# Kernel optimization log

Hardware: AMD Instinct MI355X
Metric: run time of the kernel (lower is better)

## Reference

```python
import jax, jax.numpy as jnp
import numpy as np

X_MIN, X_MAX = -3.0, 3.0
EPS = 1e-08


def setup_inputs() -> dict:
    key = jax.random.key(0)
    k1, k2, k3 = jax.random.split(key, 3)
    B, D_in, D_out, K = 8192, 512, 128, 16
    x = jax.random.normal(k1, (B, D_in), dtype=jnp.float32)
    # trunc_normal_(std=0.02) approximated by scaled normal
    weights = jax.random.normal(k2, (D_out, D_in, K), dtype=jnp.float32) * 0.02
    # xavier_uniform for skip
    limit = float(np.sqrt(6.0 / (D_in + D_out)))
    skip_w = jax.random.uniform(k3, (D_out, D_in), dtype=jnp.float32,
                                minval=-limit, maxval=limit)
    bias = jnp.zeros((D_out,), dtype=jnp.float32)
    return {"x": x, "weights": weights, "skip_w": skip_w, "bias": bias}


def reference(x, weights, skip_w, bias):
    # x: (B, D_in); weights: (D_out, D_in, K); skip_w: (D_out, D_in); bias: (D_out,)
    K = weights.shape[-1]
    t = jnp.clip((x - X_MIN) / (X_MAX - X_MIN + EPS), 0.0, 1.0)
    pos = t * (K - 1)
    idx0 = jnp.floor(pos).astype(jnp.int32)
    idx1 = jnp.minimum(idx0 + 1, K - 1)
    frac = jnp.clip(pos - idx0.astype(pos.dtype), 0.0, 1.0)
    # Hat-basis coefficients per (b, i): avoids materializing (B, D_out, D_in)
    oh0 = jax.nn.one_hot(idx0, K, dtype=x.dtype)  # (B, D_in, K)
    oh1 = jax.nn.one_hot(idx1, K, dtype=x.dtype)
    c = oh0 * (1.0 - frac)[..., None] + oh1 * frac[..., None]  # (B, D_in, K)
    # y[b,o] = sum_i (1-frac)*w[o,i,idx0] + frac*w[o,i,idx1]
    y = jnp.einsum('bik,oik->bo', c, weights)
    y = y + bias + x @ skip_w.T
    return y
```

## Files before the change

kernel.cpp:

```cpp
#include <hip/hip_runtime.h>

typedef __attribute__((ext_vector_type(8))) short short8;
typedef __attribute__((ext_vector_type(4))) float f32x4;

#define DIN 512
#define DOUT 128
#define KK 16
#define BTOT 8192
#define KAUG (DIN * KK + DIN)
#define BK 64
#define NCHUNK_TOT (KAUG / BK)
#define NSPL 8
#define CPB (NCHUNK_TOT / NSPL)
#define BM 128
#define CHUNK_BYTES (DOUT * BK * 2)
#define CBASE 32768
#define LDS_BYTES 65536

__device__ static inline unsigned short f2bf(float x) {
  unsigned u = __builtin_bit_cast(unsigned, x);
  return (unsigned short)((u + 0x7FFFu + ((u >> 16) & 1u)) >> 16);
}

__device__ static inline void llds16(const char* g, char* l) {
  __builtin_amdgcn_global_load_lds(
      (const __attribute__((address_space(1))) unsigned int*)g,
      (__attribute__((address_space(3))) unsigned int*)l, 16, 0, 0);
}

__global__ __launch_bounds__(256) void build_wpp(const float* __restrict__ w,
                                                 const float* __restrict__ sk,
                                                 unsigned short* __restrict__ wpp) {
  const int gi = blockIdx.x * 256 + threadIdx.x;
  const int g = gi >> 10;
  const int rem = gi & 1023;
  const int o = rem >> 3;
  const int kcs = rem & 7;
  const int kc = kcs ^ (o & 7);
  const int kglob = g * 64 + kc * 8;
  const float* src = (kglob < 8192) ? (w + (size_t)o * 8192 + kglob)
                                    : (sk + (size_t)o * 512 + (kglob - 8192));
  const float4 v0 = ((const float4*)src)[0];
  const float4 v1 = ((const float4*)src)[1];
  uint4 pk;
  pk.x = f2bf(v0.x) | ((unsigned)f2bf(v0.y) << 16);
  pk.y = f2bf(v0.z) | ((unsigned)f2bf(v0.w) << 16);
  pk.z = f2bf(v1.x) | ((unsigned)f2bf(v1.y) << 16);
  pk.w = f2bf(v1.z) | ((unsigned)f2bf(v1.w) << 16);
  ((uint4*)wpp)[gi] = pk;
}

__global__ __launch_bounds__(256, 2) void kan_mfma(const float* __restrict__ x,
                                                   const unsigned short* __restrict__ wpp,
                                                   const float* __restrict__ bias,
                                                   float* __restrict__ out) {
  __shared__ __align__(16) char smem[LDS_BYTES];
  const int tid = threadIdx.x;
  const int bt = blockIdx.x >> 3;
  const int sp = blockIdx.x & 7;
  const int b0 = bt * BM;
  const int wid = tid >> 6, lane = tid & 63;
  const int lr = lane & 15, lq = lane >> 4;
  const int wm = wid >> 1, wn = wid & 1;
  const int g0 = sp * CPB;

  f32x4 acc[4][4] = {};

  auto stageW = [&](int g, int buf) {
    const char* gsrc = ((const char*)wpp) + (size_t)g * CHUNK_BYTES + wid * 4096 + lane * 16;
    char* ldst = smem + buf + wid * 4096;
#pragma unroll
    for (int it = 0; it < 4; ++it) llds16(gsrc + it * 1024, ldst + it * 1024);
  };

  auto buildSpline = [&](int cbuf, float xv0, float xv1) {
#pragma unroll
    for (int hh = 0; hh < 2; ++hh) {
      const int bl = (tid >> 2) + hh * 64;
      const int il = tid & 3;
      const float xv = hh ? xv1 : xv0;
      float t = fminf(fmaxf((xv + 3.0f) * (1.0f / 6.0f), 0.0f), 1.0f);
      const float pos = t * 15.0f;
      int i0 = (int)pos;
      i0 = i0 > 14 ? 14 : i0;
      const float f = pos - (float)i0;
      char* row = smem + cbuf + bl * 128;
      const int swz = bl & 7;
      char* gA = row + (((il * 2) ^ swz) << 4);
      char* gB = row + (((il * 2 + 1) ^ swz) << 4);
      *(uint4*)gA = make_uint4(0, 0, 0, 0);
      *(uint4*)gB = make_uint4(0, 0, 0, 0);
      const unsigned short h0 = f2bf(1.0f - f);
      const unsigned short h1 = f2bf(f);
      const int i1 = i0 + 1;
      *(unsigned short*)(((i0 & 8) ? gB : gA) + (i0 & 7) * 2) = h0;
      *(unsigned short*)(((i1 & 8) ? gB : gA) + (i1 & 7) * 2) = h1;
    }
  };

  auto buildSkip = [&](int g, int cbuf) {
    const int ioff = (g - 128) * BK;
    const int bl = tid >> 1, q = tid & 1;
    const float* xr = x + (size_t)(b0 + bl) * DIN + ioff;
    char* row = smem + cbuf + bl * 128;
    const int swz = bl & 7;
#pragma unroll
    for (int gg = 0; gg < 4; ++gg) {
      const int kc = q * 4 + gg;
      const float4 v0 = ((const float4*)(xr + kc * 8))[0];
      const float4 v1 = ((const float4*)(xr + kc * 8))[1];
      uint4 pk;
      pk.x = f2bf(v0.x) | ((unsigned)f2bf(v0.y) << 16);
      pk.y = f2bf(v0.z) | ((unsigned)f2bf(v0.w) << 16);
      pk.z = f2bf(v1.x) | ((unsigned)f2bf(v1.y) << 16);
      pk.w = f2bf(v1.z) | ((unsigned)f2bf(v1.w) << 16);
      *(uint4*)(row + ((kc ^ swz) << 4)) = pk;
    }
  };

  auto loadX = [&](int g, float& a, float& b) {
    const int r0 = tid >> 2, il = tid & 3;
    a = x[(size_t)(b0 + r0) * DIN + g * 4 + il];
    b = x[(size_t)(b0 + 64 + r0) * DIN + g * 4 + il];
  };

  stageW(g0, 0);
  {
    float a, b;
    loadX(g0, a, b);
    buildSpline(CBASE + 0, a, b);
  }
  __syncthreads();

  for (int c = 0; c < CPB; ++c) {
    const int g = g0 + c;
    const int pb = (c & 1) << 14;
    const int nb = pb ^ 16384;
    const bool haveNext = (c + 1 < CPB);
    const int gn = g + 1;

    float xn0 = 0.0f, xn1 = 0.0f;
    if (haveNext && gn < 128) loadX(gn, xn0, xn1);
    if (haveNext) stageW(gn, nb);

    const char* Wb = smem + pb;
    const char* Cb = smem + CBASE + pb;
#pragma unroll
    for (int ks = 0; ks < 2; ++ks) {
      const int gq = ks * 4 + lq;
      short8 af[4], bfr[4];
#pragma unroll
      for (int mt = 0; mt < 4; ++mt) {
        const int m = wm * 64 + mt * 16 + lr;
        af[mt] = *(const short8*)(Cb + m * 128 + ((gq ^ (m & 7)) << 4));
      }
#pragma unroll
      for (int nt = 0; nt < 4; ++nt) {
        const int o = wn * 64 + nt * 16 + lr;
        bfr[nt] = *(const short8*)(Wb + o * 128 + ((gq ^ (o & 7)) << 4));
      }
#pragma unroll
      for (int mt = 0; mt < 4; ++mt)
#pragma unroll
        for (int nt = 0; nt < 4; ++nt)
          acc[mt][nt] = __builtin_amdgcn_mfma_f32_16x16x32_bf16(af[mt], bfr[nt], acc[mt][nt], 0, 0, 0);
    }

    if (haveNext) {
      if (gn < 128) buildSpline(CBASE + nb, xn0, xn1);
      else buildSkip(gn, CBASE + nb);
    }
    __syncthreads();
  }

#pragma unroll
  for (int nt = 0; nt < 4; ++nt) {
    const int col = wn * 64 + nt * 16 + lr;
    const float bv = (sp == 0) ? bias[col] : 0.0f;
#pragma unroll
    for (int mt = 0; mt < 4; ++mt) {
      const int rowb = b0 + wm * 64 + mt * 16 + lq * 4;
#pragma unroll
      for (int r = 0; r < 4; ++r)
        atomicAdd(out + (size_t)(rowb + r) * DOUT + col, acc[mt][nt][r] + bv);
    }
  }
}

__global__ void kan_naive(const float* __restrict__ x, const float* __restrict__ w,
                          const float* __restrict__ skw, const float* __restrict__ bias,
                          float* __restrict__ out) {
  const int b = blockIdx.x;
  const int o = threadIdx.x;
  float acc = bias[o];
  for (int i = 0; i < DIN; ++i) {
    float xv = x[(size_t)b * DIN + i];
    float t = fminf(fmaxf((xv + 3.0f) * (1.0f / 6.0f), 0.0f), 1.0f);
    float p = t * 15.0f;
    float fi = floorf(p);
    int i0 = (int)fi;
    int i1 = (i0 < 15) ? i0 + 1 : 15;
    float f = p - fi;
    const float* wr = &w[((size_t)o * DIN + i) * KK];
    acc += (1.0f - f) * wr[i0] + f * wr[i1] + xv * skw[(size_t)o * DIN + i];
  }
  out[(size_t)b * DOUT + o] = acc;
}

extern "C" void kernel_launch(void* const* d_in, const int* in_sizes, int n_in,
                              void* d_out, int out_size, void* d_ws, size_t ws_size,
                              hipStream_t stream) {
  const float* x    = (const float*)d_in[0];
  const float* w    = (const float*)d_in[1];
  const float* skw  = (const float*)d_in[2];
  const float* bias = (const float*)d_in[3];
  float* out = (float*)d_out;

  const size_t need = (size_t)NCHUNK_TOT * CHUNK_BYTES;
  if (ws_size < need) {
    kan_naive<<<BTOT, DOUT, 0, stream>>>(x, w, skw, bias, out);
    return;
  }

  unsigned short* wpp = (unsigned short*)d_ws;

  hipMemsetAsync(d_out, 0, (size_t)out_size * sizeof(float), stream);
  build_wpp<<<NCHUNK_TOT * 1024 / 256, 256, 0, stream>>>(w, skw, wpp);
  kan_mfma<<<(BTOT / BM) * NSPL, 256, 0, stream>>>(x, wpp, bias, out);
}
```

Before: 120.2 us.

## Load weight fragments directly from global into registers, shrink batch tile

Removes LDS staging of the weight chunk via global_load_lds. Each wave now reads its B fragments straight from a re-laid-out global buffer, with the weight layout changed to kq-major so lanes read contiguous 16-byte pieces. The batch tile is halved to 64 rows with 128-thread blocks, which doubles the block count and halves LDS use. Block order is changed so that splits sharing the same weight chunk run adjacently, and the atomic output columns are rotated per split to reduce contention. In exchange, the weights are fetched from global/L2 more often and global load latency is exposed inside the loop with no prefetch.

```diff
diff --git a/kernel.cpp b/kernel.cpp
--- a/kernel.cpp
+++ b/kernel.cpp
@@ -12,20 +12,14 @@
 #define NCHUNK_TOT (KAUG / BK)
 #define NSPL 8
 #define CPB (NCHUNK_TOT / NSPL)
-#define BM 128
+#define BM 64
 #define CHUNK_BYTES (DOUT * BK * 2)
-#define CBASE 32768
-#define LDS_BYTES 65536
+#define CT_BYTES (BM * BK * 2)
+#define LDS_BYTES (2 * CT_BYTES)
 
 __device__ static inline unsigned short f2bf(float x) {
   unsigned u = __builtin_bit_cast(unsigned, x);
   return (unsigned short)((u + 0x7FFFu + ((u >> 16) & 1u)) >> 16);
-}
-
-__device__ static inline void llds16(const char* g, char* l) {
-  __builtin_amdgcn_global_load_lds(
-      (const __attribute__((address_space(1))) unsigned int*)g,
-      (__attribute__((address_space(3))) unsigned int*)l, 16, 0, 0);
 }
 
 __global__ __launch_bounds__(256) void build_wpp(const float* __restrict__ w,
@@ -34,10 +28,9 @@
   const int gi = blockIdx.x * 256 + threadIdx.x;
   const int g = gi >> 10;
   const int rem = gi & 1023;
-  const int o = rem >> 3;
-  const int kcs = rem & 7;
-  const int kc = kcs ^ (o & 7);
-  const int kglob = g * 64 + kc * 8;
+  const int kq = rem >> 7;
+  const int o = rem & 127;
+  const int kglob = g * 64 + kq * 8;
   const float* src = (kglob < 8192) ? (w + (size_t)o * 8192 + kglob)
                                     : (sk + (size_t)o * 512 + (kglob - 8192));
   const float4 v0 = ((const float4*)src)[0];
@@ -50,33 +43,26 @@
   ((uint4*)wpp)[gi] = pk;
 }
 
-__global__ __launch_bounds__(256, 2) void kan_mfma(const float* __restrict__ x,
+__global__ __launch_bounds__(128, 2) void kan_mfma(const float* __restrict__ x,
                                                    const unsigned short* __restrict__ wpp,
                                                    const float* __restrict__ bias,
                                                    float* __restrict__ out) {
   __shared__ __align__(16) char smem[LDS_BYTES];
   const int tid = threadIdx.x;
-  const int bt = blockIdx.x >> 3;
-  const int sp = blockIdx.x & 7;
+  const int sp = blockIdx.x >> 7;
+  const int bt = blockIdx.x & 127;
   const int b0 = bt * BM;
-  const int wid = tid >> 6, lane = tid & 63;
+  const int wn = tid >> 6;
+  const int lane = tid & 63;
   const int lr = lane & 15, lq = lane >> 4;
-  const int wm = wid >> 1, wn = wid & 1;
   const int g0 = sp * CPB;
 
   f32x4 acc[4][4] = {};
 
-  auto stageW = [&](int g, int buf) {
-    const char* gsrc = ((const char*)wpp) + (size_t)g * CHUNK_BYTES + wid * 4096 + lane * 16;
-    char* ldst = smem + buf + wid * 4096;
-#pragma unroll
-    for (int it = 0; it < 4; ++it) llds16(gsrc + it * 1024, ldst + it * 1024);
-  };
-
   auto buildSpline = [&](int cbuf, float xv0, float xv1) {
 #pragma unroll
     for (int hh = 0; hh < 2; ++hh) {
-      const int bl = (tid >> 2) + hh * 64;
+      const int bl = (tid >> 2) + hh * 32;
       const int il = tid & 3;
       const float xv = hh ? xv1 : xv0;
       float t = fminf(fmaxf((xv + 3.0f) * (1.0f / 6.0f), 0.0f), 1.0f);
@@ -106,80 +92,86 @@
     const int swz = bl & 7;
 #pragma unroll
     for (int gg = 0; gg < 4; ++gg) {
-      const int kc = q * 4 + gg;
-      const float4 v0 = ((const float4*)(xr + kc * 8))[0];
-      const float4 v1 = ((const float4*)(xr + kc * 8))[1];
+      const int kq = q * 4 + gg;
+      const float4 v0 = ((const float4*)(xr + kq * 8))[0];
+      const float4 v1 = ((const float4*)(xr + kq * 8))[1];
       uint4 pk;
       pk.x = f2bf(v0.x) | ((unsigned)f2bf(v0.y) << 16);
       pk.y = f2bf(v0.z) | ((unsigned)f2bf(v0.w) << 16);
       pk.z = f2bf(v1.x) | ((unsigned)f2bf(v1.y) << 16);
       pk.w = f2bf(v1.z) | ((unsigned)f2bf(v1.w) << 16);
-      *(uint4*)(row + ((kc ^ swz) << 4)) = pk;
+      *(uint4*)(row + ((kq ^ swz) << 4)) = pk;
     }
   };
 
   auto loadX = [&](int g, float& a, float& b) {
     const int r0 = tid >> 2, il = tid & 3;
     a = x[(size_t)(b0 + r0) * DIN + g * 4 + il];
-    b = x[(size_t)(b0 + 64 + r0) * DIN + g * 4 + il];
+    b = x[(size_t)(b0 + 32 + r0) * DIN + g * 4 + il];
   };
 
-  stageW(g0, 0);
   {
     float a, b;
     loadX(g0, a, b);
-    buildSpline(CBASE + 0, a, b);
+    buildSpline(0, a, b);
   }
   __syncthreads();
 
   for (int c = 0; c < CPB; ++c) {
     const int g = g0 + c;
-    const int pb = (c & 1) << 14;
-    const int nb = pb ^ 16384;
+    const int pb = (c & 1) << 13;
+    const int nb = pb ^ 8192;
     const bool haveNext = (c + 1 < CPB);
     const int gn = g + 1;
 
+    short8 bfr[4][2];
+    {
+      const char* gb = ((const char*)wpp) + (size_t)g * CHUNK_BYTES;
+#pragma unroll
+      for (int nt = 0; nt < 4; ++nt)
+#pragma unroll
+        for (int ks = 0; ks < 2; ++ks) {
+          const int kq = ks * 4 + lq;
+          const int o = wn * 64 + nt * 16 + lr;
+          bfr[nt][ks] = *(const short8*)(gb + (size_t)((kq << 7) + o) * 16);
+        }
+    }
+
     float xn0 = 0.0f, xn1 = 0.0f;
     if (haveNext && gn < 128) loadX(gn, xn0, xn1);
-    if (haveNext) stageW(gn, nb);
-
-    const char* Wb = smem + pb;
-    const char* Cb = smem + CBASE + pb;
+
+    const char* Cb = smem + pb;
 #pragma unroll
     for (int ks = 0; ks < 2; ++ks) {
-      const int gq = ks * 4 + lq;
-      short8 af[4], bfr[4];
+      short8 af[4];
 #pragma unroll
       for (int mt = 0; mt < 4; ++mt) {
-        const int m = wm * 64 + mt * 16 + lr;
-        af[mt] = *(const short8*)(Cb + m * 128 + ((gq ^ (m & 7)) << 4));
+        const int m = mt * 16 + lr;
+        const int kq = ks * 4 + lq;
+        af[mt] = *(const short8*)(Cb + m * 128 + (((kq ^ (m & 7)) << 4)));
       }
 #pragma unroll
-      for (int nt = 0; nt < 4; ++nt) {
-        const int o = wn * 64 + nt * 16 + lr;
-        bfr[nt] = *(const short8*)(Wb + o * 128 + ((gq ^ (o & 7)) << 4));
-      }
-#pragma unroll
       for (int mt = 0; mt < 4; ++mt)
 #pragma unroll
         for (int nt = 0; nt < 4; ++nt)
-          acc[mt][nt] = __builtin_amdgcn_mfma_f32_16x16x32_bf16(af[mt], bfr[nt], acc[mt][nt], 0, 0, 0);
+          acc[mt][nt] = __builtin_amdgcn_mfma_f32_16x16x32_bf16(af[mt], bfr[nt][ks], acc[mt][nt], 0, 0, 0);
     }
 
     if (haveNext) {
-      if (gn < 128) buildSpline(CBASE + nb, xn0, xn1);
-      else buildSkip(gn, CBASE + nb);
+      if (gn < 128) buildSpline(nb, xn0, xn1);
+      else buildSkip(gn, nb);
     }
     __syncthreads();
   }
 
 #pragma unroll
-  for (int nt = 0; nt < 4; ++nt) {
+  for (int ntl = 0; ntl < 4; ++ntl) {
+    const int nt = (ntl + sp) & 3;
     const int col = wn * 64 + nt * 16 + lr;
     const float bv = (sp == 0) ? bias[col] : 0.0f;
 #pragma unroll
     for (int mt = 0; mt < 4; ++mt) {
-      const int rowb = b0 + wm * 64 + mt * 16 + lq * 4;
+      const int rowb = b0 + mt * 16 + lq * 4;
 #pragma unroll
       for (int r = 0; r < 4; ++r)
         atomicAdd(out + (size_t)(rowb + r) * DOUT + col, acc[mt][nt][r] + bv);
@@ -226,5 +218,5 @@
 
   hipMemsetAsync(d_out, 0, (size_t)out_size * sizeof(float), stream);
   build_wpp<<<NCHUNK_TOT * 1024 / 256, 256, 0, stream>>>(w, skw, wpp);
-  kan_mfma<<<(BTOT / BM) * NSPL, 256, 0, stream>>>(x, wpp, bias, out);
-}
+  kan_mfma<<<NSPL * (BTOT / BM), 128, 0, stream>>>(x, wpp, bias, out);
+}
```

Measured after the change: 298.2 us. 148% more time.
